# Kernel tuning notes

Hardware: AMD Instinct MI355X
Metric: run time of the kernel (lower is better)

Reference implementation:

```python
import jax, jax.numpy as jnp
import numpy as np

B, L, E, H = 2, 2048, 1024, 16
HD = E // H  # 64
THETA = 10000.0


def setup_inputs() -> dict:
    key = jax.random.key(0)
    ks = jax.random.split(key, 9)
    s = 1.0 / np.sqrt(E)
    return {
        "x": jax.random.normal(ks[0], (B, L, E), jnp.float32),
        "Wq": jax.random.normal(ks[1], (E, E), jnp.float32) * s,
        "bq": jax.random.normal(ks[2], (E,), jnp.float32) * 0.01,
        "Wk": jax.random.normal(ks[3], (E, E), jnp.float32) * s,
        "bk": jax.random.normal(ks[4], (E,), jnp.float32) * 0.01,
        "Wv": jax.random.normal(ks[5], (E, E), jnp.float32) * s,
        "bv": jax.random.normal(ks[6], (E,), jnp.float32) * 0.01,
        "Wo": jax.random.normal(ks[7], (E, E), jnp.float32) * s,
        "bo": jax.random.normal(ks[8], (E,), jnp.float32) * 0.01,
    }


def _rope_tables(seq_len, dim, dtype):
    # lucidrains RotaryEmbedding: inv_freq over even indices, each freq repeated twice (interleaved)
    inv_freq = 1.0 / (THETA ** (jnp.arange(0, dim, 2, dtype=jnp.float32) / dim))
    freqs = jnp.arange(seq_len, dtype=jnp.float32)[:, None] * inv_freq[None, :]  # [L, dim/2]
    freqs = jnp.repeat(freqs, 2, axis=-1)  # [L, dim] -> f0,f0,f1,f1,...
    return jnp.cos(freqs).astype(dtype), jnp.sin(freqs).astype(dtype)


def _rotate_half(x):
    # interleaved pairs (x0, x1) -> (-x1, x0)
    x2 = x.reshape(*x.shape[:-1], -1, 2)
    x2 = jnp.stack([-x2[..., 1], x2[..., 0]], axis=-1)
    return x2.reshape(x.shape)


def _apply_rope(x, cos, sin):
    # x: [B, H, L, HD]; cos/sin: [L, HD]
    return x * cos[None, None] + _rotate_half(x) * sin[None, None]


def reference(x, Wq, bq, Wk, bk, Wv, bv, Wo, bo):
    b, l, e = x.shape
    q = (x @ Wq.T + bq).reshape(b, l, H, HD).transpose(0, 2, 1, 3)
    k = (x @ Wk.T + bk).reshape(b, l, H, HD).transpose(0, 2, 1, 3)
    v = (x @ Wv.T + bv).reshape(b, l, H, HD).transpose(0, 2, 1, 3)

    cos, sin = _rope_tables(l, HD, x.dtype)
    q = _apply_rope(q, cos, sin)
    k = _apply_rope(k, cos, sin)

    scale = 1.0 / np.sqrt(HD)
    scores = jnp.einsum("bhsd,bhed->bhse", q, k) * scale  # [B,H,L,L]
    attn = jax.nn.softmax(scores, axis=-1)
    out = jnp.einsum("bhse,bhed->bhsd", attn, v)  # [B,H,L,HD]
    out = out.transpose(0, 2, 1, 3).reshape(b, l, e)
    return out @ Wo.T + bo
```

## Files before the change

### kernel.cpp

```cpp
#include <hip/hip_runtime.h>

typedef unsigned short u16;
typedef __bf16 bf16x8 __attribute__((ext_vector_type(8)));
typedef float f32x4 __attribute__((ext_vector_type(4)));

#define LOG2E 1.4426950408889634f
#define EXP2(x) __builtin_amdgcn_exp2f(x)
#define NFM (-11.0f * LOG2E)

__device__ __forceinline__ u16 f2bf(float f) {
  unsigned int u = __float_as_uint(f);
  u += 0x7fffu + ((u >> 16) & 1u);
  return (u16)(u >> 16);
}

__device__ __forceinline__ void gld16(u16* lds, const u16* g) {
  __builtin_amdgcn_global_load_lds((const __attribute__((address_space(1))) unsigned int*)g,
                                   (__attribute__((address_space(3))) unsigned int*)lds,
                                   16, 0, 0);
}

__device__ __forceinline__ bf16x8 ldsv(const u16* p) {
  return *(const bf16x8*)p;
}

union U8 { uint4 u; bf16x8 v; };

__global__ __launch_bounds__(256) void k_prep(const float* __restrict__ x,
    const float* __restrict__ wq, const float* __restrict__ wk,
    const float* __restrict__ wv, const float* __restrict__ wo,
    u16* __restrict__ xb, u16* __restrict__ wqkvb, u16* __restrict__ wob) {
  unsigned gid = blockIdx.x * 256u + threadIdx.x;
  const float4* src;
  u16* dst;
  unsigned off;
  if (gid < 1048576u)      { src = (const float4*)x;  dst = xb;              off = gid; }
  else if (gid < 1310720u) { src = (const float4*)wq; dst = wqkvb;           off = gid - 1048576u; }
  else if (gid < 1572864u) { src = (const float4*)wk; dst = wqkvb + 1048576; off = gid - 1310720u; }
  else if (gid < 1835008u) { src = (const float4*)wv; dst = wqkvb + 2097152; off = gid - 1572864u; }
  else                     { src = (const float4*)wo; dst = wob;             off = gid - 1835008u; }
  float4 f = src[off];
  ushort4 o;
  o.x = f2bf(f.x); o.y = f2bf(f.y); o.z = f2bf(f.z); o.w = f2bf(f.w);
  ((ushort4*)dst)[off] = o;
}

__global__ __launch_bounds__(256) void k_rope(float* __restrict__ cosT, float* __restrict__ sinT) {
  int t = blockIdx.x * 256 + threadIdx.x;
  int l = t >> 5, i = t & 31;
  float inv = powf(10000.0f, -(float)i * (1.0f / 32.0f));
  float ang = (float)l * inv;
  float s, c;
  sincosf(ang, &s, &c);
  cosT[t] = c;
  sinT[t] = s;
}

__device__ __forceinline__ void gemm_loop(const u16* __restrict__ A, const u16* __restrict__ B,
                                          int m0, int n0, u16* As, u16* Bs, f32x4 acc[4][4]) {
  const int tid = threadIdx.x;
  const int lane = tid & 63, wave = tid >> 6;
  const int quad = lane >> 4, l16 = lane & 15;
  const int wm = wave & 1, wn = wave >> 1;
  const int sw = l16 & 7;

#pragma unroll
  for (int i = 0; i < 4; ++i)
#pragma unroll
    for (int j = 0; j < 4; ++j)
      acc[i][j] = (f32x4){0.f, 0.f, 0.f, 0.f};

  for (int kt = 0; kt < 16; ++kt) {
    int kb = kt * 64;
#pragma unroll
    for (int it = 0; it < 4; ++it) {
      int idx = it * 256 + tid;
      int row = idx >> 3, c8 = idx & 7;
      int sc = c8 ^ (row & 7);
      gld16(As + idx * 8, A + (long)(m0 + row) * 1024 + kb + sc * 8);
      gld16(Bs + idx * 8, B + (long)(n0 + row) * 1024 + kb + sc * 8);
    }
    __syncthreads();
#pragma unroll
    for (int kk = 0; kk < 2; ++kk) {
      int ch = (kk * 4 + quad) ^ sw;
      bf16x8 a[4], b[4];
#pragma unroll
      for (int i = 0; i < 4; ++i)
        a[i] = ldsv(As + (wm * 64 + i * 16 + l16) * 64 + ch * 8);
#pragma unroll
      for (int j = 0; j < 4; ++j)
        b[j] = ldsv(Bs + (wn * 64 + j * 16 + l16) * 64 + ch * 8);
#pragma unroll
      for (int i = 0; i < 4; ++i)
#pragma unroll
        for (int j = 0; j < 4; ++j)
          acc[i][j] = __builtin_amdgcn_mfma_f32_16x16x32_bf16(a[i], b[j], acc[i][j], 0, 0, 0);
    }
    __syncthreads();
  }
}

__global__ __launch_bounds__(256) void k_qkv(const u16* __restrict__ xb, const u16* __restrict__ wqkvb,
    const float* __restrict__ bq, const float* __restrict__ bk, const float* __restrict__ bv,
    const float* __restrict__ cosT, const float* __restrict__ sinT,
    u16* __restrict__ Qg, u16* __restrict__ Kg, u16* __restrict__ VTg) {
  __shared__ __align__(16) u16 S[128 * 132];
  u16* As = S;
  u16* Bs = S + 8192;
  f32x4 acc[4][4];
  int m0 = blockIdx.y * 128, n0 = blockIdx.x * 128;
  gemm_loop(xb, wqkvb, m0, n0, As, Bs, acc);

  const int tid = threadIdx.x, lane = tid & 63, wave = tid >> 6;
  const int quad = lane >> 4, l16 = lane & 15;
  const int wm = wave & 1, wn = wave >> 1;
  const int qsel = n0 >> 10;
  const int b = m0 >> 11;
  const int mb0 = m0 & 2047;

  if (qsel < 2) {
    const float* bp = qsel ? bk : bq;
#pragma unroll
    for (int j = 0; j < 4; ++j) {
      int nl = wn * 64 + j * 16 + l16;
      int n = n0 + nl;
      int fcol = n & 1023;
      int d = fcol & 63;
      int pi = d >> 1;
      float bias = bp[fcol];
      float sgn = (d & 1) ? 1.0f : -1.0f;
#pragma unroll
      for (int i = 0; i < 4; ++i) {
#pragma unroll
        for (int r = 0; r < 4; ++r) {
          int ml = wm * 64 + i * 16 + quad * 4 + r;
          int l = mb0 + ml;
          float v = acc[i][j][r] + bias;
          float partner = __shfl_xor(v, 1);
          float c = cosT[l * 32 + pi], s = sinT[l * 32 + pi];
          float o = fmaf(v, c, sgn * partner * s);
          if (qsel == 0) o *= 0.125f;
          S[ml * 132 + nl] = f2bf(o);
        }
      }
    }
    __syncthreads();
    u16* dstb = (qsel == 0) ? Qg : Kg;
#pragma unroll
    for (int t = 0; t < 16; ++t) {
      int idx = t * 256 + tid;
      int ml = idx >> 5, c4 = idx & 31;
      int n = n0 + c4 * 4;
      int h = (n & 1023) >> 6;
      int d = n & 63;
      *(uint2*)(dstb + (((long)b * 16 + h) * 2048 + mb0 + ml) * 64 + d) =
          *(const uint2*)(S + ml * 132 + c4 * 4);
    }
  } else {
#pragma unroll
    for (int j = 0; j < 4; ++j) {
      int nl = wn * 64 + j * 16 + l16;
      float bias = bv[(n0 + nl) & 1023];
#pragma unroll
      for (int i = 0; i < 4; ++i) {
        int mb = wm * 64 + i * 16 + quad * 4;
        unsigned u0 = (unsigned)f2bf(acc[i][j][0] + bias) | ((unsigned)f2bf(acc[i][j][1] + bias) << 16);
        unsigned u1 = (unsigned)f2bf(acc[i][j][2] + bias) | ((unsigned)f2bf(acc[i][j][3] + bias) << 16);
        *(uint2*)(S + nl * 132 + mb) = make_uint2(u0, u1);
      }
    }
    __syncthreads();
#pragma unroll
    for (int t = 0; t < 16; ++t) {
      int idx = t * 256 + tid;
      int nl = idx >> 5, c4 = idx & 31;
      int vcol = (n0 & 1023) + nl;
      int h = vcol >> 6, d = vcol & 63;
      *(uint2*)(VTg + (((long)b * 16 + h) * 64 + d) * 2048 + mb0 + c4 * 4) =
          *(const uint2*)(S + nl * 132 + c4 * 4);
    }
  }
}

__global__ __launch_bounds__(256, 2) void k_attn(const u16* __restrict__ Qg, const u16* __restrict__ Kg,
    const u16* __restrict__ VTg, u16* __restrict__ Ctx) {
  __shared__ __align__(16) char smem[34816];
  u16* Ks = (u16*)smem;
  u16* Vs = (u16*)(smem + 16384);
  const int tid = threadIdx.x, lane = tid & 63, wave = tid >> 6;
  const int quad = lane >> 4, l16 = lane & 15;
  const int wm = wave & 1, wsn = wave >> 1;
  const int sw = l16 & 7;
  const int bh = blockIdx.y;
  const int m0 = blockIdx.x * 128;
  const u16* Qb = Qg + (long)bh * 2048 * 64;
  const u16* Kb = Kg + (long)bh * 2048 * 64;
  const u16* Vb = VTg + (long)bh * 64 * 2048;

  bf16x8 qf[4][2];
#pragma unroll
  for (int mt = 0; mt < 4; ++mt)
#pragma unroll
    for (int kk = 0; kk < 2; ++kk)
      qf[mt][kk] = *(const bf16x8*)(Qb + (long)(m0 + wm * 64 + mt * 16 + l16) * 64 + kk * 32 + quad * 8);

  f32x4 oacc[4][4];
  float rs[4];
#pragma unroll
  for (int dt = 0; dt < 4; ++dt)
#pragma unroll
    for (int mt = 0; mt < 4; ++mt)
      oacc[dt][mt] = (f32x4){0.f, 0.f, 0.f, 0.f};
#pragma unroll
  for (int mt = 0; mt < 4; ++mt) rs[mt] = 0.f;

  for (int st = 0; st < 16; ++st) {
    int s0 = st * 128;
#pragma unroll
    for (int it = 0; it < 4; ++it) {
      int idx = it * 256 + tid;
      int row = idx >> 3, c8 = idx & 7;
      int sc = c8 ^ (row & 7);
      gld16(Ks + idx * 8, Kb + (long)(s0 + row) * 64 + sc * 8);
    }
#pragma unroll
    for (int it = 0; it < 4; ++it) {
      int idx = it * 256 + tid;
      int row = idx >> 4, g = idx & 15;
      uint4 vv = *(const uint4*)(Vb + (long)row * 2048 + s0 + g * 8);
      u16* wp = Vs + row * 132 + g * 8;
      *(uint2*)wp = make_uint2(vv.x, vv.y);
      *(uint2*)(wp + 4) = make_uint2(vv.z, vv.w);
    }
    __syncthreads();

    f32x4 sacc[4][4];
#pragma unroll
    for (int ct = 0; ct < 4; ++ct)
#pragma unroll
      for (int mt = 0; mt < 4; ++mt)
        sacc[ct][mt] = (f32x4){0.f, 0.f, 0.f, 0.f};
#pragma unroll
    for (int kk = 0; kk < 2; ++kk) {
      int ch = (kk * 4 + quad) ^ sw;
      bf16x8 kf[4];
#pragma unroll
      for (int ct = 0; ct < 4; ++ct)
        kf[ct] = ldsv(Ks + (wsn * 64 + ct * 16 + l16) * 64 + ch * 8);
#pragma unroll
      for (int ct = 0; ct < 4; ++ct)
#pragma unroll
        for (int mt = 0; mt < 4; ++mt)
          sacc[ct][mt] = __builtin_amdgcn_mfma_f32_16x16x32_bf16(kf[ct], qf[mt][kk], sacc[ct][mt], 0, 0, 0);
    }

#pragma unroll
    for (int c = 0; c < 2; ++c) {
      unsigned pk[2][4][2];
#pragma unroll
      for (int t = 0; t < 2; ++t) {
        int ct = c * 2 + t;
#pragma unroll
        for (int mt = 0; mt < 4; ++mt) {
          unsigned b[4];
          float sum = 0.f;
#pragma unroll
          for (int r = 0; r < 4; ++r) {
            float e = EXP2(fmaf(sacc[ct][mt][r], LOG2E, NFM));
            b[r] = __float_as_uint(e);
            sum += __uint_as_float(b[r] & 0xffff0000u);
          }
          rs[mt] += sum;
          pk[t][mt][0] = __builtin_amdgcn_perm(b[1], b[0], 0x07060302u);
          pk[t][mt][1] = __builtin_amdgcn_perm(b[3], b[2], 0x07060302u);
        }
      }
#pragma unroll
      for (int dt = 0; dt < 4; ++dt) {
        const u16* vp = Vs + (dt * 16 + l16) * 132 + wsn * 64 + c * 32 + quad * 4;
        uint2 lo = *(const uint2*)vp;
        uint2 hi = *(const uint2*)(vp + 16);
        U8 vfu; vfu.u = make_uint4(lo.x, lo.y, hi.x, hi.y);
#pragma unroll
        for (int mt = 0; mt < 4; ++mt) {
          U8 pfu; pfu.u = make_uint4(pk[0][mt][0], pk[0][mt][1], pk[1][mt][0], pk[1][mt][1]);
          oacc[dt][mt] = __builtin_amdgcn_mfma_f32_16x16x32_bf16(vfu.v, pfu.v, oacc[dt][mt], 0, 0, 0);
        }
      }
    }
    __syncthreads();
  }

  float* mbuf = (float*)smem;
  if (wsn == 1) {
#pragma unroll
    for (int dt = 0; dt < 4; ++dt)
#pragma unroll
      for (int mt = 0; mt < 4; ++mt)
#pragma unroll
        for (int r = 0; r < 4; ++r)
          mbuf[(wm * 68 + dt * 16 + mt * 4 + r) * 64 + lane] = oacc[dt][mt][r];
#pragma unroll
    for (int mt = 0; mt < 4; ++mt)
      mbuf[(wm * 68 + 64 + mt) * 64 + lane] = rs[mt];
  }
  __syncthreads();
  if (wsn == 0) {
#pragma unroll
    for (int dt = 0; dt < 4; ++dt)
#pragma unroll
      for (int mt = 0; mt < 4; ++mt)
#pragma unroll
        for (int r = 0; r < 4; ++r)
          oacc[dt][mt][r] += mbuf[(wm * 68 + dt * 16 + mt * 4 + r) * 64 + lane];
#pragma unroll
    for (int mt = 0; mt < 4; ++mt) {
      rs[mt] += mbuf[(wm * 68 + 64 + mt) * 64 + lane];
      rs[mt] += __shfl_xor(rs[mt], 16);
      rs[mt] += __shfl_xor(rs[mt], 32);
    }
    const int b = bh >> 4, h = bh & 15;
#pragma unroll
    for (int mt = 0; mt < 4; ++mt) {
      float inv = 1.0f / rs[mt];
      int tok = m0 + wm * 64 + mt * 16 + l16;
      u16* cp = Ctx + ((long)(b * 2048 + tok)) * 1024 + h * 64 + quad * 4;
#pragma unroll
      for (int dt = 0; dt < 4; ++dt) {
        float o0 = oacc[dt][mt][0] * inv, o1 = oacc[dt][mt][1] * inv;
        float o2 = oacc[dt][mt][2] * inv, o3 = oacc[dt][mt][3] * inv;
        unsigned u0 = (unsigned)f2bf(o0) | ((unsigned)f2bf(o1) << 16);
        unsigned u1 = (unsigned)f2bf(o2) | ((unsigned)f2bf(o3) << 16);
        *(uint2*)(cp + dt * 16) = make_uint2(u0, u1);
      }
    }
  }
}

__global__ __launch_bounds__(256) void k_out(const u16* __restrict__ Ctx, const u16* __restrict__ wob,
    const float* __restrict__ bo, float* __restrict__ out) {
  __shared__ __align__(16) u16 As[128 * 64];
  __shared__ __align__(16) u16 Bs[128 * 64];
  f32x4 acc[4][4];
  int m0 = blockIdx.y * 128, n0 = blockIdx.x * 128;
  gemm_loop(Ctx, wob, m0, n0, As, Bs, acc);
  const int tid = threadIdx.x, lane = tid & 63, wave = tid >> 6;
  const int quad = lane >> 4, l16 = lane & 15;
  const int wm = wave & 1, wn = wave >> 1;
#pragma unroll
  for (int i = 0; i < 4; ++i)
#pragma unroll
    for (int j = 0; j < 4; ++j) {
      int n = n0 + wn * 64 + j * 16 + l16;
      float b_ = bo[n];
#pragma unroll
      for (int r = 0; r < 4; ++r) {
        int m = m0 + wm * 64 + i * 16 + quad * 4 + r;
        out[(long)m * 1024 + n] = acc[i][j][r] + b_;
      }
    }
}

extern "C" void kernel_launch(void* const* d_in, const int* in_sizes, int n_in,
                              void* d_out, int out_size, void* d_ws, size_t ws_size,
                              hipStream_t stream) {
  const float* x  = (const float*)d_in[0];
  const float* Wq = (const float*)d_in[1];
  const float* bq = (const float*)d_in[2];
  const float* Wk = (const float*)d_in[3];
  const float* bk = (const float*)d_in[4];
  const float* Wv = (const float*)d_in[5];
  const float* bv = (const float*)d_in[6];
  const float* Wo = (const float*)d_in[7];
  const float* bo = (const float*)d_in[8];
  float* out = (float*)d_out;

  char* ws = (char*)d_ws;
  u16* xb    = (u16*)(ws);
  u16* wqkvb = (u16*)(ws + (8ul << 20));
  u16* wob   = (u16*)(ws + (14ul << 20));
  u16* Qg    = (u16*)(ws + (16ul << 20));
  u16* Kg    = (u16*)(ws + (24ul << 20));
  u16* VTg   = (u16*)(ws + (32ul << 20));
  u16* Ctx   = (u16*)(ws + (40ul << 20));
  float* cosT = (float*)(ws + (48ul << 20));
  float* sinT = (float*)(ws + (48ul << 20) + (256ul << 10));

  k_prep<<<dim3(8192), dim3(256), 0, stream>>>(x, Wq, Wk, Wv, Wo, xb, wqkvb, wob);
  k_rope<<<dim3(256), dim3(256), 0, stream>>>(cosT, sinT);
  k_qkv<<<dim3(24, 32), dim3(256), 0, stream>>>(xb, wqkvb, bq, bk, bv, cosT, sinT, Qg, Kg, VTg);
  k_attn<<<dim3(16, 32), dim3(256), 0, stream>>>(Qg, Kg, VTg, Ctx);
  k_out<<<dim3(8, 32), dim3(256), 0, stream>>>(Ctx, wob, bo, out);
}
```

Baseline: 213.8 us.

## Double-buffer GEMM LDS tiles and fold RoPE table build into prep kernel

The shared GEMM loop now stages the next K-tile into a second LDS buffer while MFMAs run on the current one. This removes one barrier per iteration and overlaps global-to-LDS loads with compute. LDS per block doubles to 64KB in the QKV and output GEMMs, which may lower occupancy. Separately, the cos/sin table computation is merged into the bf16 conversion kernel as extra blocks, saving a kernel launch.

```diff
diff --git a/kernel.cpp b/kernel.cpp
--- a/kernel.cpp
+++ b/kernel.cpp
@@ -29,8 +29,20 @@
 __global__ __launch_bounds__(256) void k_prep(const float* __restrict__ x,
     const float* __restrict__ wq, const float* __restrict__ wk,
     const float* __restrict__ wv, const float* __restrict__ wo,
-    u16* __restrict__ xb, u16* __restrict__ wqkvb, u16* __restrict__ wob) {
+    u16* __restrict__ xb, u16* __restrict__ wqkvb, u16* __restrict__ wob,
+    float* __restrict__ cosT, float* __restrict__ sinT) {
   unsigned gid = blockIdx.x * 256u + threadIdx.x;
+  if (gid >= 2097152u) {
+    unsigned t = gid - 2097152u;
+    int l = t >> 5, i = t & 31;
+    float inv = powf(10000.0f, -(float)i * (1.0f / 32.0f));
+    float ang = (float)l * inv;
+    float s, c;
+    sincosf(ang, &s, &c);
+    cosT[t] = c;
+    sinT[t] = s;
+    return;
+  }
   const float4* src;
   u16* dst;
   unsigned off;
@@ -45,19 +57,21 @@
   ((ushort4*)dst)[off] = o;
 }
 
-__global__ __launch_bounds__(256) void k_rope(float* __restrict__ cosT, float* __restrict__ sinT) {
-  int t = blockIdx.x * 256 + threadIdx.x;
-  int l = t >> 5, i = t & 31;
-  float inv = powf(10000.0f, -(float)i * (1.0f / 32.0f));
-  float ang = (float)l * inv;
-  float s, c;
-  sincosf(ang, &s, &c);
-  cosT[t] = c;
-  sinT[t] = s;
+__device__ __forceinline__ void stage_tile(const u16* __restrict__ A, const u16* __restrict__ B,
+                                           int m0, int n0, int kb, u16* dst) {
+  const int tid = threadIdx.x;
+#pragma unroll
+  for (int it = 0; it < 4; ++it) {
+    int idx = it * 256 + tid;
+    int row = idx >> 3, c8 = idx & 7;
+    int sc = c8 ^ (row & 7);
+    gld16(dst + idx * 8,        A + (long)(m0 + row) * 1024 + kb + sc * 8);
+    gld16(dst + 8192 + idx * 8, B + (long)(n0 + row) * 1024 + kb + sc * 8);
+  }
 }
 
 __device__ __forceinline__ void gemm_loop(const u16* __restrict__ A, const u16* __restrict__ B,
-                                          int m0, int n0, u16* As, u16* Bs, f32x4 acc[4][4]) {
+                                          int m0, int n0, u16* S, f32x4 acc[4][4]) {
   const int tid = threadIdx.x;
   const int lane = tid & 63, wave = tid >> 6;
   const int quad = lane >> 4, l16 = lane & 15;
@@ -70,17 +84,15 @@
     for (int j = 0; j < 4; ++j)
       acc[i][j] = (f32x4){0.f, 0.f, 0.f, 0.f};
 
+  stage_tile(A, B, m0, n0, 0, S);
+  __syncthreads();
+
   for (int kt = 0; kt < 16; ++kt) {
-    int kb = kt * 64;
-#pragma unroll
-    for (int it = 0; it < 4; ++it) {
-      int idx = it * 256 + tid;
-      int row = idx >> 3, c8 = idx & 7;
-      int sc = c8 ^ (row & 7);
-      gld16(As + idx * 8, A + (long)(m0 + row) * 1024 + kb + sc * 8);
-      gld16(Bs + idx * 8, B + (long)(n0 + row) * 1024 + kb + sc * 8);
-    }
-    __syncthreads();
+    const int off = (kt & 1) << 14;
+    const u16* As = S + off;
+    const u16* Bs = S + off + 8192;
+    if (kt < 15)
+      stage_tile(A, B, m0, n0, (kt + 1) * 64, S + (off ^ 16384));
 #pragma unroll
     for (int kk = 0; kk < 2; ++kk) {
       int ch = (kk * 4 + quad) ^ sw;
@@ -105,12 +117,10 @@
     const float* __restrict__ bq, const float* __restrict__ bk, const float* __restrict__ bv,
     const float* __restrict__ cosT, const float* __restrict__ sinT,
     u16* __restrict__ Qg, u16* __restrict__ Kg, u16* __restrict__ VTg) {
-  __shared__ __align__(16) u16 S[128 * 132];
-  u16* As = S;
-  u16* Bs = S + 8192;
+  __shared__ __align__(16) u16 S[32768];
   f32x4 acc[4][4];
   int m0 = blockIdx.y * 128, n0 = blockIdx.x * 128;
-  gemm_loop(xb, wqkvb, m0, n0, As, Bs, acc);
+  gemm_loop(xb, wqkvb, m0, n0, S, acc);
 
   const int tid = threadIdx.x, lane = tid & 63, wave = tid >> 6;
   const int quad = lane >> 4, l16 = lane & 15;
@@ -340,11 +350,10 @@
 
 __global__ __launch_bounds__(256) void k_out(const u16* __restrict__ Ctx, const u16* __restrict__ wob,
     const float* __restrict__ bo, float* __restrict__ out) {
-  __shared__ __align__(16) u16 As[128 * 64];
-  __shared__ __align__(16) u16 Bs[128 * 64];
+  __shared__ __align__(16) u16 S[32768];
   f32x4 acc[4][4];
   int m0 = blockIdx.y * 128, n0 = blockIdx.x * 128;
-  gemm_loop(Ctx, wob, m0, n0, As, Bs, acc);
+  gemm_loop(Ctx, wob, m0, n0, S, acc);
   const int tid = threadIdx.x, lane = tid & 63, wave = tid >> 6;
   const int quad = lane >> 4, l16 = lane & 15;
   const int wm = wave & 1, wn = wave >> 1;
@@ -387,8 +396,7 @@
   float* cosT = (float*)(ws + (48ul << 20));
   float* sinT = (float*)(ws + (48ul << 20) + (256ul << 10));
 
-  k_prep<<<dim3(8192), dim3(256), 0, stream>>>(x, Wq, Wk, Wv, Wo, xb, wqkvb, wob);
-  k_rope<<<dim3(256), dim3(256), 0, stream>>>(cosT, sinT);
+  k_prep<<<dim3(8448), dim3(256), 0, stream>>>(x, Wq, Wk, Wv, Wo, xb, wqkvb, wob, cosT, sinT);
   k_qkv<<<dim3(24, 32), dim3(256), 0, stream>>>(xb, wqkvb, bq, bk, bv, cosT, sinT, Qg, Kg, VTg);
   k_attn<<<dim3(16, 32), dim3(256), 0, stream>>>(Qg, Kg, VTg, Ctx);
   k_out<<<dim3(8, 32), dim3(256), 0, stream>>>(Ctx, wob, bo, out);
```

Result: faster. 202.7 us (-5.2%).
